# Kernel optimization log

Measured on AMD Instinct MI355X. Metric: run time of the kernel, lower is better.

Reference implementation:

```python
import jax, jax.numpy as jnp
import numpy as np

IN_FEATURES = 4096
OUT_FEATURES = 11008
BATCH = 2048


def setup_inputs() -> dict:
    key = jax.random.key(0)
    k1, k2, k3, k4 = jax.random.split(key, 4)
    # int8-range activations, stored as int32 for exact integer accumulation
    input = jax.random.randint(k1, (BATCH, IN_FEATURES), -127, 128, dtype=jnp.int32)
    # ternary weights in {-1, 0, 1}
    ternary_weight = jax.random.randint(k2, (OUT_FEATURES, IN_FEATURES), -1, 2, dtype=jnp.int32)
    weight_scale = jax.random.uniform(k3, (OUT_FEATURES, 1), dtype=jnp.float32, minval=0.01, maxval=0.1)
    bias = jax.random.normal(k4, (OUT_FEATURES,), dtype=jnp.float32) * 0.01
    return {"input": input, "ternary_weight": ternary_weight,
            "weight_scale": weight_scale, "bias": bias}


def reference(input, ternary_weight, weight_scale, bias):
    # Equivalent to the per-column add/sub loop: int32 accumulate of
    # input @ ternary_weight.T, since w in {-1,0,1}.
    acc = jnp.einsum('bi,oi->bo', input, ternary_weight)  # int32 [B, O]
    out = acc.astype(jnp.float32) * weight_scale.reshape(1, -1)
    out = out + bias
    return out
```

## Files before the change

kernel.cpp:

```cpp
#include <hip/hip_runtime.h>
#include <stdint.h>

#define BATCH   2048
#define KDIM    4096
#define NDIM    11008

#define BM 128
#define BN 256
#define BK 64
#define NT (KDIM / BK)
#define ABYTES (BM * BK)
#define BBYTES (BN * BK)
#define BUF_BYTES (ABYTES + BBYTES)
#define A_OFF 0
#define B_OFF ABYTES

typedef __attribute__((ext_vector_type(4))) int i32x4;

typedef const __attribute__((address_space(1))) char glob_char;
typedef __attribute__((address_space(3))) char lds_char;

__device__ __forceinline__ unsigned pack4(i32x4 v) {
  return  ((unsigned)v.x & 0xFFu)
        | (((unsigned)v.y & 0xFFu) << 8)
        | (((unsigned)v.z & 0xFFu) << 16)
        | (((unsigned)v.w)         << 24);
}

__global__ __launch_bounds__(256) void convert_i32_i8(const int* __restrict__ src,
                                                      unsigned* __restrict__ dst,
                                                      int n4) {
  int idx = blockIdx.x * 256 + threadIdx.x;
  if (idx >= n4) return;
  i32x4 v = ((const i32x4*)src)[idx];
  dst[idx] = pack4(v);
}

__global__ __launch_bounds__(512, 4) void ternary_gemm(const char* __restrict__ A8,
                                                       const char* __restrict__ B8,
                                                       const float* __restrict__ scale,
                                                       const float* __restrict__ bias,
                                                       float* __restrict__ out) {
  __shared__ char lds[3 * BUF_BYTES];

  const int tid  = threadIdx.x;
  const int wid  = tid >> 6;
  const int lane = tid & 63;

  const int nwg = gridDim.x;
  const int cpx = nwg >> 3;
  const int wg  = (blockIdx.x & 7) * cpx + (blockIdx.x >> 3);
  const int mt = wg & 15;
  const int nt = wg >> 4;
  const int arow0 = mt * BM;
  const int brow0 = nt * BN;

  const int wr = wid >> 2;
  const int wc = wid & 3;
  const int rsub = lane & 15;
  const int sgrp = lane >> 4;

  const int srow  = tid >> 2;
  const int sslot = (tid & 3) ^ ((srow >> 1) & 3);
  const char* gA  = A8 + (size_t)(arow0 + srow) * KDIM + sslot * 16;
  const char* gB0 = B8 + (size_t)(brow0 + srow) * KDIM + sslot * 16;
  const char* gB1 = B8 + (size_t)(brow0 + 128 + srow) * KDIM + sslot * 16;

  auto stageA = [&](int bufo, int kt) {
    __builtin_amdgcn_global_load_lds((glob_char*)(gA + kt * BK),
        (lds_char*)(lds + bufo + A_OFF + wid * 1024), 16, 0, 0);
  };
  auto stageB = [&](int bufo, int kt, int r) {
    const char* g = (r == 0) ? gB0 : gB1;
    __builtin_amdgcn_global_load_lds((glob_char*)(g + kt * BK),
        (lds_char*)(lds + bufo + B_OFF + r * 8192 + wid * 1024), 16, 0, 0);
  };

  int offA[4], offB[4];
#pragma unroll
  for (int m = 0; m < 4; ++m) {
    const int row = wr * 64 + m * 16 + rsub;
    const int p   = sgrp ^ ((row >> 1) & 3);
    offA[m] = A_OFF + row * 64 + p * 16;
  }
#pragma unroll
  for (int n = 0; n < 4; ++n) {
    const int row = wc * 64 + n * 16 + rsub;
    const int p   = sgrp ^ ((row >> 1) & 3);
    offB[n] = B_OFF + row * 64 + p * 16;
  }

  i32x4 acc[4][4];
#pragma unroll
  for (int m = 0; m < 4; ++m)
#pragma unroll
    for (int n = 0; n < 4; ++n)
      acc[m][n] = (i32x4){0, 0, 0, 0};

  int cur = 0, nxt = BUF_BYTES, pf = 2 * BUF_BYTES;

  stageB(cur, 0, 0); stageB(cur, 0, 1); stageA(cur, 0);
  stageB(nxt, 1, 0); stageB(nxt, 1, 1); stageA(nxt, 1);
  asm volatile("s_waitcnt vmcnt(3)" ::: "memory");
  __builtin_amdgcn_s_barrier();

  for (int t = 0; t < NT; ++t) {
    const int kt2 = (t + 2 < NT) ? t + 2 : NT - 1;

    i32x4 a0, a1, a2, a3, b0, b1, b2, b3;

    a0 = *(const i32x4*)(lds + cur + offA[0]);
    a1 = *(const i32x4*)(lds + cur + offA[1]);
    b0 = *(const i32x4*)(lds + cur + offB[0]);
    b1 = *(const i32x4*)(lds + cur + offB[1]);
    stageB(pf, kt2, 0);
    __builtin_amdgcn_s_barrier();
    __builtin_amdgcn_s_setprio(1);
    acc[0][0] = __builtin_amdgcn_mfma_i32_16x16x64_i8(a0, b0, acc[0][0], 0, 0, 0);
    acc[0][1] = __builtin_amdgcn_mfma_i32_16x16x64_i8(a0, b1, acc[0][1], 0, 0, 0);
    acc[1][0] = __builtin_amdgcn_mfma_i32_16x16x64_i8(a1, b0, acc[1][0], 0, 0, 0);
    acc[1][1] = __builtin_amdgcn_mfma_i32_16x16x64_i8(a1, b1, acc[1][1], 0, 0, 0);
    __builtin_amdgcn_s_setprio(0);
    __builtin_amdgcn_s_barrier();

    b2 = *(const i32x4*)(lds + cur + offB[2]);
    b3 = *(const i32x4*)(lds + cur + offB[3]);
    stageB(pf, kt2, 1);
    __builtin_amdgcn_s_barrier();
    __builtin_amdgcn_s_setprio(1);
    acc[0][2] = __builtin_amdgcn_mfma_i32_16x16x64_i8(a0, b2, acc[0][2], 0, 0, 0);
    acc[0][3] = __builtin_amdgcn_mfma_i32_16x16x64_i8(a0, b3, acc[0][3], 0, 0, 0);
    acc[1][2] = __builtin_amdgcn_mfma_i32_16x16x64_i8(a1, b2, acc[1][2], 0, 0, 0);
    acc[1][3] = __builtin_amdgcn_mfma_i32_16x16x64_i8(a1, b3, acc[1][3], 0, 0, 0);
    __builtin_amdgcn_s_setprio(0);
    __builtin_amdgcn_s_barrier();

    a2 = *(const i32x4*)(lds + cur + offA[2]);
    a3 = *(const i32x4*)(lds + cur + offA[3]);
    stageA(pf, kt2);
    __builtin_amdgcn_s_barrier();
    __builtin_amdgcn_s_setprio(1);
    acc[2][2] = __builtin_amdgcn_mfma_i32_16x16x64_i8(a2, b2, acc[2][2], 0, 0, 0);
    acc[2][3] = __builtin_amdgcn_mfma_i32_16x16x64_i8(a2, b3, acc[2][3], 0, 0, 0);
    acc[3][2] = __builtin_amdgcn_mfma_i32_16x16x64_i8(a3, b2, acc[3][2], 0, 0, 0);
    acc[3][3] = __builtin_amdgcn_mfma_i32_16x16x64_i8(a3, b3, acc[3][3], 0, 0, 0);
    __builtin_amdgcn_s_setprio(0);
    __builtin_amdgcn_s_barrier();

    asm volatile("s_waitcnt vmcnt(3)" ::: "memory");
    __builtin_amdgcn_s_barrier();
    __builtin_amdgcn_s_setprio(1);
    acc[2][0] = __builtin_amdgcn_mfma_i32_16x16x64_i8(a2, b0, acc[2][0], 0, 0, 0);
    acc[2][1] = __builtin_amdgcn_mfma_i32_16x16x64_i8(a2, b1, acc[2][1], 0, 0, 0);
    acc[3][0] = __builtin_amdgcn_mfma_i32_16x16x64_i8(a3, b0, acc[3][0], 0, 0, 0);
    acc[3][1] = __builtin_amdgcn_mfma_i32_16x16x64_i8(a3, b1, acc[3][1], 0, 0, 0);
    __builtin_amdgcn_s_setprio(0);
    __builtin_amdgcn_s_barrier();

    const int tb = cur; cur = nxt; nxt = pf; pf = tb;
  }

  const int crow = sgrp * 4;
#pragma unroll
  for (int n = 0; n < 4; ++n) {
    const int col = brow0 + wc * 64 + n * 16 + rsub;
    const float sc = scale[col];
    const float bs = bias[col];
#pragma unroll
    for (int m = 0; m < 4; ++m) {
      const int r0 = arow0 + wr * 64 + m * 16 + crow;
#pragma unroll
      for (int j = 0; j < 4; ++j) {
        out[(size_t)(r0 + j) * NDIM + col] = (float)acc[m][n][j] * sc + bs;
      }
    }
  }
}

extern "C" void kernel_launch(void* const* d_in, const int* in_sizes, int n_in,
                              void* d_out, int out_size, void* d_ws, size_t ws_size,
                              hipStream_t stream) {
  const int*   input  = (const int*)d_in[0];
  const int*   weight = (const int*)d_in[1];
  const float* scale  = (const float*)d_in[2];
  const float* bias   = (const float*)d_in[3];
  float*       out    = (float*)d_out;

  const size_t needA = (size_t)BATCH * KDIM;
  const size_t needB = (size_t)NDIM * KDIM;

  char* A8 = (char*)d_ws;
  char* B8 = A8 + needA;
  const int nA4 = (int)(needA / 4);
  const int nB4 = (int)(needB / 4);
  convert_i32_i8<<<(nA4 + 255) / 256, 256, 0, stream>>>(input, (unsigned*)A8, nA4);
  convert_i32_i8<<<(nB4 + 255) / 256, 256, 0, stream>>>(weight, (unsigned*)B8, nB4);

  const dim3 grid((BATCH / BM) * (NDIM / BN));
  const dim3 block(512);
  ternary_gemm<<<grid, block, 0, stream>>>(A8, B8, scale, bias, out);
  (void)ws_size; (void)n_in; (void)in_sizes; (void)out_size;
}
```

Baseline: 156.2 us.

## Use 4 waves per block with 64x128 per-wave tiles in ternary GEMM

Halves the threads per block to 256 and gives each wave a 64x128 output sub-tile (4x8 MFMA accumulators) instead of 64x64. The global-to-LDS staging is reorganised so each thread issues six async loads per k-step, and the wait counts are adjusted to match. The aim is more register-level reuse of A and B fragments and fewer LDS reads per MFMA. The cost is higher register pressure and fewer resident waves to hide memory latency.

```diff
diff --git a/kernel.cpp b/kernel.cpp
--- a/kernel.cpp
+++ b/kernel.cpp
@@ -36,7 +36,7 @@
   dst[idx] = pack4(v);
 }
 
-__global__ __launch_bounds__(512, 4) void ternary_gemm(const char* __restrict__ A8,
+__global__ __launch_bounds__(256, 2) void ternary_gemm(const char* __restrict__ A8,
                                                        const char* __restrict__ B8,
                                                        const float* __restrict__ scale,
                                                        const float* __restrict__ bias,
@@ -55,28 +55,26 @@
   const int arow0 = mt * BM;
   const int brow0 = nt * BN;
 
-  const int wr = wid >> 2;
-  const int wc = wid & 3;
+  const int wr = wid >> 1;
+  const int wc = wid & 1;
   const int rsub = lane & 15;
   const int sgrp = lane >> 4;
 
   const int srow  = tid >> 2;
   const int sslot = (tid & 3) ^ ((srow >> 1) & 3);
-  const char* gA  = A8 + (size_t)(arow0 + srow) * KDIM + sslot * 16;
-  const char* gB0 = B8 + (size_t)(brow0 + srow) * KDIM + sslot * 16;
-  const char* gB1 = B8 + (size_t)(brow0 + 128 + srow) * KDIM + sslot * 16;
-
-  auto stageA = [&](int bufo, int kt) {
-    __builtin_amdgcn_global_load_lds((glob_char*)(gA + kt * BK),
-        (lds_char*)(lds + bufo + A_OFF + wid * 1024), 16, 0, 0);
+  const char* gA0 = A8 + (size_t)(arow0       + srow) * KDIM + sslot * 16;
+  const char* gA1 = A8 + (size_t)(arow0 +  64 + srow) * KDIM + sslot * 16;
+  const char* gB0 = B8 + (size_t)(brow0       + srow) * KDIM + sslot * 16;
+  const char* gB1 = B8 + (size_t)(brow0 +  64 + srow) * KDIM + sslot * 16;
+  const char* gB2 = B8 + (size_t)(brow0 + 128 + srow) * KDIM + sslot * 16;
+  const char* gB3 = B8 + (size_t)(brow0 + 192 + srow) * KDIM + sslot * 16;
+
+  auto stage = [&](const char* g, int bufo, int kt, int dsto) {
+    __builtin_amdgcn_global_load_lds((glob_char*)(g + kt * BK),
+        (lds_char*)(lds + bufo + dsto + wid * 1024), 16, 0, 0);
   };
-  auto stageB = [&](int bufo, int kt, int r) {
-    const char* g = (r == 0) ? gB0 : gB1;
-    __builtin_amdgcn_global_load_lds((glob_char*)(g + kt * BK),
-        (lds_char*)(lds + bufo + B_OFF + r * 8192 + wid * 1024), 16, 0, 0);
-  };
-
-  int offA[4], offB[4];
+
+  int offA[4], offB[8];
 #pragma unroll
   for (int m = 0; m < 4; ++m) {
     const int row = wr * 64 + m * 16 + rsub;
@@ -84,86 +82,113 @@
     offA[m] = A_OFF + row * 64 + p * 16;
   }
 #pragma unroll
-  for (int n = 0; n < 4; ++n) {
-    const int row = wc * 64 + n * 16 + rsub;
+  for (int n = 0; n < 8; ++n) {
+    const int row = wc * 128 + n * 16 + rsub;
     const int p   = sgrp ^ ((row >> 1) & 3);
     offB[n] = B_OFF + row * 64 + p * 16;
   }
 
-  i32x4 acc[4][4];
+  i32x4 acc[4][8];
 #pragma unroll
   for (int m = 0; m < 4; ++m)
 #pragma unroll
-    for (int n = 0; n < 4; ++n)
+    for (int n = 0; n < 8; ++n)
       acc[m][n] = (i32x4){0, 0, 0, 0};
 
   int cur = 0, nxt = BUF_BYTES, pf = 2 * BUF_BYTES;
 
-  stageB(cur, 0, 0); stageB(cur, 0, 1); stageA(cur, 0);
-  stageB(nxt, 1, 0); stageB(nxt, 1, 1); stageA(nxt, 1);
-  asm volatile("s_waitcnt vmcnt(3)" ::: "memory");
+  stage(gB0, cur, 0, B_OFF);         stage(gB1, cur, 0, B_OFF + 4096);
+  stage(gB2, cur, 0, B_OFF + 8192);  stage(gB3, cur, 0, B_OFF + 12288);
+  stage(gA0, cur, 0, A_OFF);         stage(gA1, cur, 0, A_OFF + 4096);
+  stage(gB0, nxt, 1, B_OFF);         stage(gB1, nxt, 1, B_OFF + 4096);
+  stage(gB2, nxt, 1, B_OFF + 8192);  stage(gB3, nxt, 1, B_OFF + 12288);
+  stage(gA0, nxt, 1, A_OFF);         stage(gA1, nxt, 1, A_OFF + 4096);
+  asm volatile("s_waitcnt vmcnt(6)" ::: "memory");
   __builtin_amdgcn_s_barrier();
 
   for (int t = 0; t < NT; ++t) {
     const int kt2 = (t + 2 < NT) ? t + 2 : NT - 1;
 
-    i32x4 a0, a1, a2, a3, b0, b1, b2, b3;
+    i32x4 a0, a1, a2, a3, b0, b1, b2, b3, b4, b5, b6, b7;
 
     a0 = *(const i32x4*)(lds + cur + offA[0]);
     a1 = *(const i32x4*)(lds + cur + offA[1]);
     b0 = *(const i32x4*)(lds + cur + offB[0]);
     b1 = *(const i32x4*)(lds + cur + offB[1]);
-    stageB(pf, kt2, 0);
+    b2 = *(const i32x4*)(lds + cur + offB[2]);
+    b3 = *(const i32x4*)(lds + cur + offB[3]);
+    stage(gB0, pf, kt2, B_OFF);
+    stage(gB1, pf, kt2, B_OFF + 4096);
     __builtin_amdgcn_s_barrier();
     __builtin_amdgcn_s_setprio(1);
     acc[0][0] = __builtin_amdgcn_mfma_i32_16x16x64_i8(a0, b0, acc[0][0], 0, 0, 0);
     acc[0][1] = __builtin_amdgcn_mfma_i32_16x16x64_i8(a0, b1, acc[0][1], 0, 0, 0);
+    acc[0][2] = __builtin_amdgcn_mfma_i32_16x16x64_i8(a0, b2, acc[0][2], 0, 0, 0);
+    acc[0][3] = __builtin_amdgcn_mfma_i32_16x16x64_i8(a0, b3, acc[0][3], 0, 0, 0);
     acc[1][0] = __builtin_amdgcn_mfma_i32_16x16x64_i8(a1, b0, acc[1][0], 0, 0, 0);
     acc[1][1] = __builtin_amdgcn_mfma_i32_16x16x64_i8(a1, b1, acc[1][1], 0, 0, 0);
-    __builtin_amdgcn_s_setprio(0);
-    __builtin_amdgcn_s_barrier();
-
-    b2 = *(const i32x4*)(lds + cur + offB[2]);
-    b3 = *(const i32x4*)(lds + cur + offB[3]);
-    stageB(pf, kt2, 1);
-    __builtin_amdgcn_s_barrier();
-    __builtin_amdgcn_s_setprio(1);
-    acc[0][2] = __builtin_amdgcn_mfma_i32_16x16x64_i8(a0, b2, acc[0][2], 0, 0, 0);
-    acc[0][3] = __builtin_amdgcn_mfma_i32_16x16x64_i8(a0, b3, acc[0][3], 0, 0, 0);
     acc[1][2] = __builtin_amdgcn_mfma_i32_16x16x64_i8(a1, b2, acc[1][2], 0, 0, 0);
     acc[1][3] = __builtin_amdgcn_mfma_i32_16x16x64_i8(a1, b3, acc[1][3], 0, 0, 0);
     __builtin_amdgcn_s_setprio(0);
     __builtin_amdgcn_s_barrier();
 
+    b4 = *(const i32x4*)(lds + cur + offB[4]);
+    b5 = *(const i32x4*)(lds + cur + offB[5]);
+    b6 = *(const i32x4*)(lds + cur + offB[6]);
+    b7 = *(const i32x4*)(lds + cur + offB[7]);
+    stage(gB2, pf, kt2, B_OFF + 8192);
+    stage(gB3, pf, kt2, B_OFF + 12288);
+    __builtin_amdgcn_s_barrier();
+    __builtin_amdgcn_s_setprio(1);
+    acc[0][4] = __builtin_amdgcn_mfma_i32_16x16x64_i8(a0, b4, acc[0][4], 0, 0, 0);
+    acc[0][5] = __builtin_amdgcn_mfma_i32_16x16x64_i8(a0, b5, acc[0][5], 0, 0, 0);
+    acc[0][6] = __builtin_amdgcn_mfma_i32_16x16x64_i8(a0, b6, acc[0][6], 0, 0, 0);
+    acc[0][7] = __builtin_amdgcn_mfma_i32_16x16x64_i8(a0, b7, acc[0][7], 0, 0, 0);
+    acc[1][4] = __builtin_amdgcn_mfma_i32_16x16x64_i8(a1, b4, acc[1][4], 0, 0, 0);
+    acc[1][5] = __builtin_amdgcn_mfma_i32_16x16x64_i8(a1, b5, acc[1][5], 0, 0, 0);
+    acc[1][6] = __builtin_amdgcn_mfma_i32_16x16x64_i8(a1, b6, acc[1][6], 0, 0, 0);
+    acc[1][7] = __builtin_amdgcn_mfma_i32_16x16x64_i8(a1, b7, acc[1][7], 0, 0, 0);
+    __builtin_amdgcn_s_setprio(0);
+    __builtin_amdgcn_s_barrier();
+
     a2 = *(const i32x4*)(lds + cur + offA[2]);
     a3 = *(const i32x4*)(lds + cur + offA[3]);
-    stageA(pf, kt2);
-    __builtin_amdgcn_s_barrier();
-    __builtin_amdgcn_s_setprio(1);
+    stage(gA0, pf, kt2, A_OFF);
+    stage(gA1, pf, kt2, A_OFF + 4096);
+    __builtin_amdgcn_s_barrier();
+    __builtin_amdgcn_s_setprio(1);
+    acc[2][4] = __builtin_amdgcn_mfma_i32_16x16x64_i8(a2, b4, acc[2][4], 0, 0, 0);
+    acc[2][5] = __builtin_amdgcn_mfma_i32_16x16x64_i8(a2, b5, acc[2][5], 0, 0, 0);
+    acc[2][6] = __builtin_amdgcn_mfma_i32_16x16x64_i8(a2, b6, acc[2][6], 0, 0, 0);
+    acc[2][7] = __builtin_amdgcn_mfma_i32_16x16x64_i8(a2, b7, acc[2][7], 0, 0, 0);
+    acc[3][4] = __builtin_amdgcn_mfma_i32_16x16x64_i8(a3, b4, acc[3][4], 0, 0, 0);
+    acc[3][5] = __builtin_amdgcn_mfma_i32_16x16x64_i8(a3, b5, acc[3][5], 0, 0, 0);
+    acc[3][6] = __builtin_amdgcn_mfma_i32_16x16x64_i8(a3, b6, acc[3][6], 0, 0, 0);
+    acc[3][7] = __builtin_amdgcn_mfma_i32_16x16x64_i8(a3, b7, acc[3][7], 0, 0, 0);
+    __builtin_amdgcn_s_setprio(0);
+    __builtin_amdgcn_s_barrier();
+
+    asm volatile("s_waitcnt vmcnt(6)" ::: "memory");
+    __builtin_amdgcn_s_barrier();
+    __builtin_amdgcn_s_setprio(1);
+    acc[2][0] = __builtin_amdgcn_mfma_i32_16x16x64_i8(a2, b0, acc[2][0], 0, 0, 0);
+    acc[2][1] = __builtin_amdgcn_mfma_i32_16x16x64_i8(a2, b1, acc[2][1], 0, 0, 0);
     acc[2][2] = __builtin_amdgcn_mfma_i32_16x16x64_i8(a2, b2, acc[2][2], 0, 0, 0);
     acc[2][3] = __builtin_amdgcn_mfma_i32_16x16x64_i8(a2, b3, acc[2][3], 0, 0, 0);
+    acc[3][0] = __builtin_amdgcn_mfma_i32_16x16x64_i8(a3, b0, acc[3][0], 0, 0, 0);
+    acc[3][1] = __builtin_amdgcn_mfma_i32_16x16x64_i8(a3, b1, acc[3][1], 0, 0, 0);
     acc[3][2] = __builtin_amdgcn_mfma_i32_16x16x64_i8(a3, b2, acc[3][2], 0, 0, 0);
     acc[3][3] = __builtin_amdgcn_mfma_i32_16x16x64_i8(a3, b3, acc[3][3], 0, 0, 0);
     __builtin_amdgcn_s_setprio(0);
     __builtin_amdgcn_s_barrier();
 
-    asm volatile("s_waitcnt vmcnt(3)" ::: "memory");
-    __builtin_amdgcn_s_barrier();
-    __builtin_amdgcn_s_setprio(1);
-    acc[2][0] = __builtin_amdgcn_mfma_i32_16x16x64_i8(a2, b0, acc[2][0], 0, 0, 0);
-    acc[2][1] = __builtin_amdgcn_mfma_i32_16x16x64_i8(a2, b1, acc[2][1], 0, 0, 0);
-    acc[3][0] = __builtin_amdgcn_mfma_i32_16x16x64_i8(a3, b0, acc[3][0], 0, 0, 0);
-    acc[3][1] = __builtin_amdgcn_mfma_i32_16x16x64_i8(a3, b1, acc[3][1], 0, 0, 0);
-    __builtin_amdgcn_s_setprio(0);
-    __builtin_amdgcn_s_barrier();
-
     const int tb = cur; cur = nxt; nxt = pf; pf = tb;
   }
 
   const int crow = sgrp * 4;
 #pragma unroll
-  for (int n = 0; n < 4; ++n) {
-    const int col = brow0 + wc * 64 + n * 16 + rsub;
+  for (int n = 0; n < 8; ++n) {
+    const int col = brow0 + wc * 128 + n * 16 + rsub;
     const float sc = scale[col];
     const float bs = bias[col];
 #pragma unroll
@@ -197,7 +222,7 @@
   convert_i32_i8<<<(nB4 + 255) / 256, 256, 0, stream>>>(weight, (unsigned*)B8, nB4);
 
   const dim3 grid((BATCH / BM) * (NDIM / BN));
-  const dim3 block(512);
+  const dim3 block(256);
   ternary_gemm<<<grid, block, 0, stream>>>(A8, B8, scale, bias, out);
   (void)ws_size; (void)n_in; (void)in_sizes; (void)out_size;
 }
```

Result: no change. 155.4 us (-0.5%).

## Shrink GEMM tile to 128x128 with 4-wave blocks and two-phase MFMA schedule

Applied to the files above, without the earlier changes.

Halves the N tile to 128 and runs 256-thread blocks, where each of 4 waves computes a 64x64 sub-tile. Both A halves and both B halves are staged with one generic global-to-LDS helper. The per-k-step schedule drops from four barrier-separated MFMA groups to two groups of eight, with explicit lgkmcnt waits and sched_barriers. The intent is fewer barriers per step, smaller LDS per block so more blocks fit per CU, and better tail balance across the larger grid. The cost is lower arithmetic intensity per tile, which means more global and L2 traffic for the operands.

```diff
diff --git a/kernel.cpp b/kernel.cpp
--- a/kernel.cpp
+++ b/kernel.cpp
@@ -6,7 +6,7 @@
 #define NDIM    11008
 
 #define BM 128
-#define BN 256
+#define BN 128
 #define BK 64
 #define NT (KDIM / BK)
 #define ABYTES (BM * BK)
@@ -36,7 +36,7 @@
   dst[idx] = pack4(v);
 }
 
-__global__ __launch_bounds__(512, 4) void ternary_gemm(const char* __restrict__ A8,
+__global__ __launch_bounds__(256, 3) void ternary_gemm(const char* __restrict__ A8,
                                                        const char* __restrict__ B8,
                                                        const float* __restrict__ scale,
                                                        const float* __restrict__ bias,
@@ -55,25 +55,21 @@
   const int arow0 = mt * BM;
   const int brow0 = nt * BN;
 
-  const int wr = wid >> 2;
-  const int wc = wid & 3;
+  const int wr = wid >> 1;
+  const int wc = wid & 1;
   const int rsub = lane & 15;
   const int sgrp = lane >> 4;
 
   const int srow  = tid >> 2;
   const int sslot = (tid & 3) ^ ((srow >> 1) & 3);
-  const char* gA  = A8 + (size_t)(arow0 + srow) * KDIM + sslot * 16;
-  const char* gB0 = B8 + (size_t)(brow0 + srow) * KDIM + sslot * 16;
-  const char* gB1 = B8 + (size_t)(brow0 + 128 + srow) * KDIM + sslot * 16;
+  const char* gA0 = A8 + (size_t)(arow0      + srow) * KDIM + sslot * 16;
+  const char* gA1 = A8 + (size_t)(arow0 + 64 + srow) * KDIM + sslot * 16;
+  const char* gB0 = B8 + (size_t)(brow0      + srow) * KDIM + sslot * 16;
+  const char* gB1 = B8 + (size_t)(brow0 + 64 + srow) * KDIM + sslot * 16;
 
-  auto stageA = [&](int bufo, int kt) {
-    __builtin_amdgcn_global_load_lds((glob_char*)(gA + kt * BK),
-        (lds_char*)(lds + bufo + A_OFF + wid * 1024), 16, 0, 0);
-  };
-  auto stageB = [&](int bufo, int kt, int r) {
-    const char* g = (r == 0) ? gB0 : gB1;
+  auto stage = [&](const char* g, int bufo, int kt, int dsto) {
     __builtin_amdgcn_global_load_lds((glob_char*)(g + kt * BK),
-        (lds_char*)(lds + bufo + B_OFF + r * 8192 + wid * 1024), 16, 0, 0);
+        (lds_char*)(lds + bufo + dsto + wid * 1024), 16, 0, 0);
   };
 
   int offA[4], offB[4];
@@ -99,9 +95,11 @@
 
   int cur = 0, nxt = BUF_BYTES, pf = 2 * BUF_BYTES;
 
-  stageB(cur, 0, 0); stageB(cur, 0, 1); stageA(cur, 0);
-  stageB(nxt, 1, 0); stageB(nxt, 1, 1); stageA(nxt, 1);
-  asm volatile("s_waitcnt vmcnt(3)" ::: "memory");
+  stage(gA0, cur, 0, A_OFF);  stage(gA1, cur, 0, A_OFF + 4096);
+  stage(gB0, cur, 0, B_OFF);  stage(gB1, cur, 0, B_OFF + 4096);
+  stage(gA0, nxt, 1, A_OFF);  stage(gA1, nxt, 1, A_OFF + 4096);
+  stage(gB0, nxt, 1, B_OFF);  stage(gB1, nxt, 1, B_OFF + 4096);
+  asm volatile("s_waitcnt vmcnt(4)" ::: "memory");
   __builtin_amdgcn_s_barrier();
 
   for (int t = 0; t < NT; ++t) {
@@ -111,49 +109,44 @@
 
     a0 = *(const i32x4*)(lds + cur + offA[0]);
     a1 = *(const i32x4*)(lds + cur + offA[1]);
+    a2 = *(const i32x4*)(lds + cur + offA[2]);
+    a3 = *(const i32x4*)(lds + cur + offA[3]);
     b0 = *(const i32x4*)(lds + cur + offB[0]);
     b1 = *(const i32x4*)(lds + cur + offB[1]);
-    stageB(pf, kt2, 0);
+    stage(gA0, pf, kt2, A_OFF);
+    stage(gA1, pf, kt2, A_OFF + 4096);
     __builtin_amdgcn_s_barrier();
+    asm volatile("s_waitcnt lgkmcnt(0)" ::: "memory");
+    __builtin_amdgcn_sched_barrier(0);
     __builtin_amdgcn_s_setprio(1);
     acc[0][0] = __builtin_amdgcn_mfma_i32_16x16x64_i8(a0, b0, acc[0][0], 0, 0, 0);
+    acc[1][0] = __builtin_amdgcn_mfma_i32_16x16x64_i8(a1, b0, acc[1][0], 0, 0, 0);
+    acc[2][0] = __builtin_amdgcn_mfma_i32_16x16x64_i8(a2, b0, acc[2][0], 0, 0, 0);
+    acc[3][0] = __builtin_amdgcn_mfma_i32_16x16x64_i8(a3, b0, acc[3][0], 0, 0, 0);
     acc[0][1] = __builtin_amdgcn_mfma_i32_16x16x64_i8(a0, b1, acc[0][1], 0, 0, 0);
-    acc[1][0] = __builtin_amdgcn_mfma_i32_16x16x64_i8(a1, b0, acc[1][0], 0, 0, 0);
     acc[1][1] = __builtin_amdgcn_mfma_i32_16x16x64_i8(a1, b1, acc[1][1], 0, 0, 0);
+    acc[2][1] = __builtin_amdgcn_mfma_i32_16x16x64_i8(a2, b1, acc[2][1], 0, 0, 0);
+    acc[3][1] = __builtin_amdgcn_mfma_i32_16x16x64_i8(a3, b1, acc[3][1], 0, 0, 0);
     __builtin_amdgcn_s_setprio(0);
     __builtin_amdgcn_s_barrier();
 
     b2 = *(const i32x4*)(lds + cur + offB[2]);
     b3 = *(const i32x4*)(lds + cur + offB[3]);
-    stageB(pf, kt2, 1);
+    stage(gB0, pf, kt2, B_OFF);
+    stage(gB1, pf, kt2, B_OFF + 4096);
+    asm volatile("s_waitcnt vmcnt(4)" ::: "memory");
     __builtin_amdgcn_s_barrier();
+    asm volatile("s_waitcnt lgkmcnt(0)" ::: "memory");
+    __builtin_amdgcn_sched_barrier(0);
     __builtin_amdgcn_s_setprio(1);
     acc[0][2] = __builtin_amdgcn_mfma_i32_16x16x64_i8(a0, b2, acc[0][2], 0, 0, 0);
+    acc[1][2] = __builtin_amdgcn_mfma_i32_16x16x64_i8(a1, b2, acc[1][2], 0, 0, 0);
+    acc[2][2] = __builtin_amdgcn_mfma_i32_16x16x64_i8(a2, b2, acc[2][2], 0, 0, 0);
+    acc[3][2] = __builtin_amdgcn_mfma_i32_16x16x64_i8(a3, b2, acc[3][2], 0, 0, 0);
     acc[0][3] = __builtin_amdgcn_mfma_i32_16x16x64_i8(a0, b3, acc[0][3], 0, 0, 0);
-    acc[1][2] = __builtin_amdgcn_mfma_i32_16x16x64_i8(a1, b2, acc[1][2], 0, 0, 0);
     acc[1][3] = __builtin_amdgcn_mfma_i32_16x16x64_i8(a1, b3, acc[1][3], 0, 0, 0);
-    __builtin_amdgcn_s_setprio(0);
-    __builtin_amdgcn_s_barrier();
-
-    a2 = *(const i32x4*)(lds + cur + offA[2]);
-    a3 = *(const i32x4*)(lds + cur + offA[3]);
-    stageA(pf, kt2);
-    __builtin_amdgcn_s_barrier();
-    __builtin_amdgcn_s_setprio(1);
-    acc[2][2] = __builtin_amdgcn_mfma_i32_16x16x64_i8(a2, b2, acc[2][2], 0, 0, 0);
     acc[2][3] = __builtin_amdgcn_mfma_i32_16x16x64_i8(a2, b3, acc[2][3], 0, 0, 0);
-    acc[3][2] = __builtin_amdgcn_mfma_i32_16x16x64_i8(a3, b2, acc[3][2], 0, 0, 0);
     acc[3][3] = __builtin_amdgcn_mfma_i32_16x16x64_i8(a3, b3, acc[3][3], 0, 0, 0);
-    __builtin_amdgcn_s_setprio(0);
-    __builtin_amdgcn_s_barrier();
-
-    asm volatile("s_waitcnt vmcnt(3)" ::: "memory");
-    __builtin_amdgcn_s_barrier();
-    __builtin_amdgcn_s_setprio(1);
-    acc[2][0] = __builtin_amdgcn_mfma_i32_16x16x64_i8(a2, b0, acc[2][0], 0, 0, 0);
-    acc[2][1] = __builtin_amdgcn_mfma_i32_16x16x64_i8(a2, b1, acc[2][1], 0, 0, 0);
-    acc[3][0] = __builtin_amdgcn_mfma_i32_16x16x64_i8(a3, b0, acc[3][0], 0, 0, 0);
-    acc[3][1] = __builtin_amdgcn_mfma_i32_16x16x64_i8(a3, b1, acc[3][1], 0, 0, 0);
     __builtin_amdgcn_s_setprio(0);
     __builtin_amdgcn_s_barrier();
 
@@ -197,7 +190,7 @@
   convert_i32_i8<<<(nB4 + 255) / 256, 256, 0, stream>>>(weight, (unsigned*)B8, nB4);
 
   const dim3 grid((BATCH / BM) * (NDIM / BN));
-  const dim3 block(512);
+  const dim3 block(256);
   ternary_gemm<<<grid, block, 0, stream>>>(A8, B8, scale, bias, out);
   (void)ws_size; (void)n_in; (void)in_sizes; (void)out_size;
 }
```

Result: slower. 174.1 us (+11.5%).
